# Performance work log

Hardware: AMD Instinct MI355X
Metric: run time of the kernel (lower is better)

## Reference

```python
import jax, jax.numpy as jnp
import numpy as np

EPS = 1e-5  # BatchNorm eps


def _add_self_loops(edge_index, num_nodes):
    loop = jnp.arange(num_nodes, dtype=edge_index.dtype)
    src = jnp.concatenate([edge_index[0], loop])
    dst = jnp.concatenate([edge_index[1], loop])
    return src, dst


def _gcn_conv(x, src, dst, norm, W, b, num_nodes):
    # PyG GCNConv: out = D^{-1/2} (A+I) D^{-1/2} (x W) + b
    h = x @ W                                # [N, out_dim]
    msg = h[src] * norm[:, None]             # [E+N, out_dim] gathered messages
    out = jax.ops.segment_sum(msg, dst, num_segments=num_nodes)
    return out + b


def _batch_norm(x, gamma, beta):
    # training-mode batch statistics over the node dimension (biased var)
    mean = jnp.mean(x, axis=0)
    var = jnp.var(x, axis=0)
    return (x - mean) * jax.lax.rsqrt(var + EPS) * gamma + beta


def setup_inputs() -> dict:
    key = jax.random.key(0)
    ks = jax.random.split(key, 10)
    N, E = 50000, 800000
    d_in, d_h, d_mid, d_out = 1536, 512, 128, 5

    x = jax.random.normal(ks[0], (N, d_in), dtype=jnp.float32)
    edge_index = jax.random.randint(ks[1], (2, E), 0, N, dtype=jnp.int32)

    def glorot(k, fan_in, fan_out):
        s = jnp.sqrt(6.0 / (fan_in + fan_out))
        return jax.random.uniform(k, (fan_in, fan_out), jnp.float32, -s, s)

    return {
        "x": x,
        "edge_index": edge_index,
        "W1": glorot(ks[2], d_in, d_h), "b1": jnp.zeros((d_h,), jnp.float32),
        "W2": glorot(ks[3], d_h, d_mid), "b2": jnp.zeros((d_mid,), jnp.float32),
        "W3": glorot(ks[4], d_mid, d_out), "b3": jnp.zeros((d_out,), jnp.float32),
        "gamma1": jnp.ones((d_h,), jnp.float32), "beta1": jnp.zeros((d_h,), jnp.float32),
        "gamma2": jnp.ones((d_mid,), jnp.float32), "beta2": jnp.zeros((d_mid,), jnp.float32),
    }


def reference(x, edge_index, W1, b1, W2, b2, W3, b3, gamma1, beta1, gamma2, beta2):
    N = x.shape[0]
    src, dst = _add_self_loops(edge_index, N)
    # symmetric degree normalization deg^{-1/2}[src] * deg^{-1/2}[dst]
    deg = jax.ops.segment_sum(jnp.ones_like(dst, dtype=x.dtype), dst, num_segments=N)
    inv_sqrt = jnp.where(deg > 0, jax.lax.rsqrt(deg), 0.0)
    norm = inv_sqrt[src] * inv_sqrt[dst]

    h = _gcn_conv(x, src, dst, norm, W1, b1, N)
    h = jax.nn.relu(_batch_norm(h, gamma1, beta1))  # dropout is identity in eval
    h = _gcn_conv(h, src, dst, norm, W2, b2, N)
    h = jax.nn.relu(_batch_norm(h, gamma2, beta2))
    h = _gcn_conv(h, src, dst, norm, W3, b3, N)
    return jax.nn.log_softmax(h, axis=1)
```

## Files before the change

kernel.cpp:

```cpp
#include <hip/hip_runtime.h>
#include <cstddef>
#include <cstdint>

typedef short s16x8 __attribute__((ext_vector_type(8)));
typedef unsigned short u16x4 __attribute__((ext_vector_type(4)));
typedef unsigned short u16x8 __attribute__((ext_vector_type(8)));
typedef float f32x4 __attribute__((ext_vector_type(4)));

__device__ __forceinline__ unsigned short f2bf(float f) {
  unsigned int u = __float_as_uint(f);
  u = (u + 0x7fffu + ((u >> 16) & 1u)) >> 16;
  return (unsigned short)u;
}
__device__ __forceinline__ float bf2f(unsigned short u) {
  return __uint_as_float(((unsigned int)u) << 16);
}

__device__ __forceinline__ void gl2lds16(const unsigned short* g, unsigned short* l) {
  __builtin_amdgcn_global_load_lds(
      (const __attribute__((address_space(1))) unsigned int*)g,
      (__attribute__((address_space(3))) unsigned int*)l, 16, 0, 0);
}
__device__ __forceinline__ void gl2lds16f(const float* g, float* l) {
  __builtin_amdgcn_global_load_lds(
      (const __attribute__((address_space(1))) unsigned int*)g,
      (__attribute__((address_space(3))) unsigned int*)l, 16, 0, 0);
}

static inline size_t alignup(size_t x) { return (x + 255) & ~(size_t)255; }

__global__ void count_kernel(const int* __restrict__ dst, int* __restrict__ counts, int E) {
  int e = blockIdx.x * blockDim.x + threadIdx.x;
  if (e < E) atomicAdd(&counts[dst[e]], 1);
}

__global__ void invsqrt_kernel(const int* __restrict__ counts, float* __restrict__ inv_s, int n) {
  int i = blockIdx.x * blockDim.x + threadIdx.x;
  if (i < n) inv_s[i] = rsqrtf((float)(counts[i] + 1));
}

__global__ void block_sum_kernel(const int* __restrict__ counts, int* __restrict__ bsum, int n) {
  __shared__ int red[256];
  int i = blockIdx.x * 256 + threadIdx.x;
  red[threadIdx.x] = (i < n) ? counts[i] : 0;
  __syncthreads();
  #pragma unroll
  for (int o = 128; o > 0; o >>= 1) {
    if (threadIdx.x < o) red[threadIdx.x] += red[threadIdx.x + o];
    __syncthreads();
  }
  if (threadIdx.x == 0) bsum[blockIdx.x] = red[0];
}

__global__ void scan_bsum_kernel(int* __restrict__ bsum, int nb) {
  __shared__ int s[256];
  int t = threadIdx.x;
  s[t] = (t < nb) ? bsum[t] : 0;
  __syncthreads();
  #pragma unroll
  for (int o = 1; o < 256; o <<= 1) {
    int v = (t >= o) ? s[t - o] : 0;
    __syncthreads();
    s[t] += v;
    __syncthreads();
  }
  if (t < nb) bsum[t] = (t == 0) ? 0 : s[t - 1];
}

__global__ void scan_apply_kernel(const int* __restrict__ counts, const int* __restrict__ bpre,
                                  int* __restrict__ offsets, int n) {
  __shared__ int s[256];
  int t = threadIdx.x;
  int i = blockIdx.x * 256 + t;
  s[t] = (i < n) ? counts[i] : 0;
  __syncthreads();
  #pragma unroll
  for (int o = 1; o < 256; o <<= 1) {
    int v = (t >= o) ? s[t - o] : 0;
    __syncthreads();
    s[t] += v;
    __syncthreads();
  }
  if (i < n) offsets[i + 1] = s[t] + bpre[blockIdx.x];
  if (i == 0) offsets[0] = 0;
}

__global__ void fill_kernel(const int* __restrict__ src, const int* __restrict__ dst,
                            const int* __restrict__ offsets, int* __restrict__ cursor,
                            int* __restrict__ csr_src, int E) {
  int e = blockIdx.x * blockDim.x + threadIdx.x;
  if (e >= E) return;
  int d = dst[e];
  int pos = atomicAdd(&cursor[d], 1);
  csr_src[offsets[d] + pos] = src[e];
}

__global__ void transpose_w_kernel(const float* __restrict__ W, unsigned short* __restrict__ Wt,
                                   int K, int N) {
  __shared__ float tile[32][33];
  int k0 = blockIdx.x * 32, n0 = blockIdx.y * 32;
  int tx = threadIdx.x & 31, ty = threadIdx.x >> 5;
  #pragma unroll
  for (int i = 0; i < 32; i += 8)
    tile[ty + i][tx] = W[(size_t)(k0 + ty + i) * N + n0 + tx];
  __syncthreads();
  #pragma unroll
  for (int i = 0; i < 32; i += 8)
    Wt[(size_t)(n0 + ty + i) * K + k0 + tx] = f2bf(tile[tx][ty + i]);
}

__global__ __launch_bounds__(512) void gemm1_kernel(
    const float* __restrict__ A, const unsigned short* __restrict__ B,
    unsigned short* __restrict__ C, int M) {
  __shared__ __align__(16) float As[2][128 * 32];
  __shared__ __align__(16) unsigned short Bs[2][256 * 32];
  const int K = 1536;
  const int NT = 48;
  int tid = threadIdx.x, lane = tid & 63, w = tid >> 6;

  int nwg = gridDim.x * gridDim.y;
  int orig = blockIdx.y * gridDim.x + blockIdx.x;
  int q = nwg >> 3, r = nwg & 7;
  int xcd = orig & 7, loc = orig >> 3;
  int wg = (xcd < r) ? xcd * (q + 1) + loc : r * (q + 1) + (xcd - r) * q + loc;
  int bx = wg & 1, by = wg >> 1;

  int m0 = by * 128, n0 = bx * 256;
  int wm = (w >> 2) * 64, wn = (w & 3) * 64;

  f32x4 acc[4][4];
  #pragma unroll
  for (int i = 0; i < 4; i++)
    #pragma unroll
    for (int j = 0; j < 4; j++) acc[i][j] = (f32x4){0.f, 0.f, 0.f, 0.f};

  int row0 = tid >> 3, slot0 = tid & 7;
  int row1 = 64 + row0;
  const float* agp0 = &A[(size_t)min(m0 + row0, M - 1) * K + ((slot0 ^ (row0 & 7)) << 2)];
  const float* agp1 = &A[(size_t)min(m0 + row1, M - 1) * K + ((slot0 ^ (row1 & 7)) << 2)];
  int adst0 = tid * 4, adst1 = (512 + tid) * 4;
  int brow = tid >> 2, bslot = tid & 3;
  int bsrc = (bslot ^ (brow & 3)) << 3;
  const unsigned short* bgp0 = &B[(size_t)(n0 + brow) * K + bsrc];
  const unsigned short* bgp1 = &B[(size_t)(n0 + 128 + brow) * K + bsrc];
  int bdst0 = tid * 8, bdst1 = (512 + tid) * 8;

  gl2lds16f(agp0, &As[0][adst0]);
  gl2lds16f(agp1, &As[0][adst1]);
  gl2lds16(bgp0, &Bs[0][bdst0]);
  gl2lds16(bgp1, &Bs[0][bdst1]);
  __syncthreads();

  int cur = 0;
  for (int t = 0; t < NT; t++) {
    if (t + 1 < NT) {
      int kb = (t + 1) * 32;
      gl2lds16f(agp0 + kb, &As[cur ^ 1][adst0]);
      gl2lds16f(agp1 + kb, &As[cur ^ 1][adst1]);
      gl2lds16(bgp0 + kb, &Bs[cur ^ 1][bdst0]);
      gl2lds16(bgp1 + kb, &Bs[cur ^ 1][bdst1]);
    }
    int jc = lane >> 4;
    s16x8 af[4], bfr[4];
    #pragma unroll
    for (int i = 0; i < 4; i++) {
      int rr = wm + i * 16 + (lane & 15);
      f32x4 v0 = *reinterpret_cast<const f32x4*>(
          &As[cur][rr * 32 + ((((2 * jc) ^ (rr & 7))) << 2)]);
      f32x4 v1 = *reinterpret_cast<const f32x4*>(
          &As[cur][rr * 32 + ((((2 * jc + 1) ^ (rr & 7))) << 2)]);
      unsigned int c0, c1, c2, c3;
      asm("v_cvt_pk_bf16_f32 %0, %1, %2" : "=v"(c0) : "v"(v0[0]), "v"(v0[1]));
      asm("v_cvt_pk_bf16_f32 %0, %1, %2" : "=v"(c1) : "v"(v0[2]), "v"(v0[3]));
      asm("v_cvt_pk_bf16_f32 %0, %1, %2" : "=v"(c2) : "v"(v1[0]), "v"(v1[1]));
      asm("v_cvt_pk_bf16_f32 %0, %1, %2" : "=v"(c3) : "v"(v1[2]), "v"(v1[3]));
      uint4 pk;
      pk.x = c0; pk.y = c1; pk.z = c2; pk.w = c3;
      af[i] = __builtin_bit_cast(s16x8, pk);
      int rn = wn + i * 16 + (lane & 15);
      bfr[i] = *reinterpret_cast<const s16x8*>(&Bs[cur][rn * 32 + ((jc ^ (rn & 3)) << 3)]);
    }
    #pragma unroll
    for (int i = 0; i < 4; i++)
      #pragma unroll
      for (int j = 0; j < 4; j++)
        acc[i][j] = __builtin_amdgcn_mfma_f32_16x16x32_bf16(af[i], bfr[j], acc[i][j], 0, 0, 0);
    __syncthreads();
    cur ^= 1;
  }

  #pragma unroll
  for (int i = 0; i < 4; i++) {
    #pragma unroll
    for (int j = 0; j < 4; j++) {
      int col = n0 + wn + j * 16 + (lane & 15);
      #pragma unroll
      for (int r2 = 0; r2 < 4; r2++) {
        int row = m0 + wm + i * 16 + (lane >> 4) * 4 + r2;
        if (row < M) C[(size_t)row * 512 + col] = f2bf(acc[i][j][r2]);
      }
    }
  }
}

#define LDT 72
__global__ __launch_bounds__(256) void gemm2_kernel(
    const unsigned short* __restrict__ A, const unsigned short* __restrict__ Bt,
    const float* __restrict__ sc, const float* __restrict__ sh,
    unsigned short* __restrict__ C, int M) {
  const int N = 128, K = 512;
  __shared__ unsigned short As[64 * LDT];
  __shared__ unsigned short Bs[128 * LDT];
  int tid = threadIdx.x;
  int m0 = blockIdx.y * 64;
  int w = tid >> 6, lane = tid & 63;
  int wm = (w >> 1) * 32, wn = (w & 1) * 64;

  f32x4 acc[2][4];
  #pragma unroll
  for (int i = 0; i < 2; i++)
    #pragma unroll
    for (int j = 0; j < 4; j++) acc[i][j] = (f32x4){0.f, 0.f, 0.f, 0.f};

  for (int k0 = 0; k0 < K; k0 += 64) {
    #pragma unroll
    for (int r = 0; r < 2; r++) {
      int idx = r * 256 + tid;
      int row = idx >> 3;
      int seg = (idx & 7) * 8;
      int gr = m0 + row;
      u16x8 v = (u16x8){0, 0, 0, 0, 0, 0, 0, 0};
      if (gr < M) v = *reinterpret_cast<const u16x8*>(&A[(size_t)gr * K + k0 + seg]);
      int c = k0 + seg;
      u16x8 p;
      #pragma unroll
      for (int j = 0; j < 8; j++) {
        float f = fmaxf(bf2f(v[j]) * sc[c + j] + sh[c + j], 0.f);
        p[j] = f2bf(f);
      }
      *reinterpret_cast<u16x8*>(&As[row * LDT + seg]) = p;
    }
    #pragma unroll
    for (int r = 0; r < 4; r++) {
      int idx = r * 256 + tid;
      int n = idx >> 3;
      int seg = (idx & 7) * 8;
      u16x8 v = *reinterpret_cast<const u16x8*>(&Bt[(size_t)n * K + k0 + seg]);
      *reinterpret_cast<u16x8*>(&Bs[n * LDT + seg]) = v;
    }
    __syncthreads();
    #pragma unroll
    for (int ks = 0; ks < 2; ks++) {
      s16x8 af[2], bfr[4];
      #pragma unroll
      for (int i = 0; i < 2; i++)
        af[i] = *reinterpret_cast<const s16x8*>(
            &As[(wm + i * 16 + (lane & 15)) * LDT + ks * 32 + (lane >> 4) * 8]);
      #pragma unroll
      for (int j = 0; j < 4; j++)
        bfr[j] = *reinterpret_cast<const s16x8*>(
            &Bs[(wn + j * 16 + (lane & 15)) * LDT + ks * 32 + (lane >> 4) * 8]);
      #pragma unroll
      for (int i = 0; i < 2; i++)
        #pragma unroll
        for (int j = 0; j < 4; j++)
          acc[i][j] = __builtin_amdgcn_mfma_f32_16x16x32_bf16(af[i], bfr[j], acc[i][j], 0, 0, 0);
    }
    __syncthreads();
  }
  #pragma unroll
  for (int i = 0; i < 2; i++) {
    #pragma unroll
    for (int j = 0; j < 4; j++) {
      int col = wn + j * 16 + (lane & 15);
      #pragma unroll
      for (int r = 0; r < 4; r++) {
        int row = m0 + wm + i * 16 + (lane >> 4) * 4 + r;
        if (row < M) C[(size_t)row * N + col] = f2bf(acc[i][j][r]);
      }
    }
  }
}

__global__ void agg512_kernel(const unsigned short* __restrict__ h, const int* __restrict__ offsets,
                              const int* __restrict__ csr, const float* __restrict__ inv_s,
                              unsigned short* __restrict__ out, int n) {
  int wv = threadIdx.x >> 6, lane = threadIdx.x & 63;
  int node = blockIdx.x * 4 + wv;
  if (node >= n) return;
  const u16x8* h8 = reinterpret_cast<const u16x8*>(h);
  float di = inv_s[node];
  size_t rb = (size_t)node * 64;
  float acc[8];
  u16x8 v0 = h8[rb + lane];
  float dd = di * di;
  #pragma unroll
  for (int j = 0; j < 8; j++) acc[j] = bf2f(v0[j]) * dd;
  int e = offsets[node], e1 = offsets[node + 1];
  for (; e + 1 < e1; e += 2) {
    int sA = csr[e], sB = csr[e + 1];
    float wA = inv_s[sA] * di, wB = inv_s[sB] * di;
    u16x8 vA = h8[(size_t)sA * 64 + lane];
    u16x8 vB = h8[(size_t)sB * 64 + lane];
    #pragma unroll
    for (int j = 0; j < 8; j++) acc[j] += bf2f(vA[j]) * wA + bf2f(vB[j]) * wB;
  }
  if (e < e1) {
    int sA = csr[e];
    float wA = inv_s[sA] * di;
    u16x8 vA = h8[(size_t)sA * 64 + lane];
    #pragma unroll
    for (int j = 0; j < 8; j++) acc[j] += bf2f(vA[j]) * wA;
  }
  u16x8 o;
  #pragma unroll
  for (int j = 0; j < 8; j++) o[j] = f2bf(acc[j]);
  reinterpret_cast<u16x8*>(out)[rb + lane] = o;
}

__global__ void agg128_kernel(const unsigned short* __restrict__ h, const int* __restrict__ offsets,
                              const int* __restrict__ csr, const float* __restrict__ inv_s,
                              unsigned short* __restrict__ out, int n) {
  int wv = threadIdx.x >> 6, lane = threadIdx.x & 63;
  int node = blockIdx.x * 4 + wv;
  if (node >= n) return;
  const unsigned int* h2 = reinterpret_cast<const unsigned int*>(h);
  float di = inv_s[node];
  size_t rb = (size_t)node * 64;
  unsigned int u0 = h2[rb + lane];
  float dd = di * di;
  float alo = __uint_as_float(u0 << 16) * dd;
  float ahi = __uint_as_float(u0 & 0xffff0000u) * dd;
  int e = offsets[node], e1 = offsets[node + 1];
  for (; e + 1 < e1; e += 2) {
    int sA = csr[e], sB = csr[e + 1];
    float wA = inv_s[sA] * di, wB = inv_s[sB] * di;
    unsigned int uA = h2[(size_t)sA * 64 + lane];
    unsigned int uB = h2[(size_t)sB * 64 + lane];
    alo += __uint_as_float(uA << 16) * wA + __uint_as_float(uB << 16) * wB;
    ahi += __uint_as_float(uA & 0xffff0000u) * wA + __uint_as_float(uB & 0xffff0000u) * wB;
  }
  if (e < e1) {
    int sA = csr[e];
    float wA = inv_s[sA] * di;
    unsigned int uA = h2[(size_t)sA * 64 + lane];
    alo += __uint_as_float(uA << 16) * wA;
    ahi += __uint_as_float(uA & 0xffff0000u) * wA;
  }
  unsigned int uo = ((unsigned int)f2bf(ahi) << 16) | (unsigned int)f2bf(alo);
  reinterpret_cast<unsigned int*>(out)[rb + lane] = uo;
}

__global__ void bn_stats512_kernel(const unsigned short* __restrict__ x, float* __restrict__ accum,
                                   int nrows, int rpb) {
  int r0 = blockIdx.x * rpb, r1 = min(nrows, r0 + rpb);
  int t = threadIdx.x;
  const unsigned int* x2 = reinterpret_cast<const unsigned int*>(x);
  float s0 = 0.f, q0 = 0.f, s1 = 0.f, q1 = 0.f;
  for (int r = r0; r < r1; r++) {
    unsigned int u = x2[(size_t)r * 256 + t];
    float lo = __uint_as_float(u << 16);
    float hi = __uint_as_float(u & 0xffff0000u);
    s0 += lo; q0 += lo * lo; s1 += hi; q1 += hi * hi;
  }
  atomicAdd(&accum[2 * t], s0);
  atomicAdd(&accum[2 * t + 1], s1);
  atomicAdd(&accum[512 + 2 * t], q0);
  atomicAdd(&accum[512 + 2 * t + 1], q1);
}

__global__ void bn_stats128_kernel(const unsigned short* __restrict__ x, float* __restrict__ accum,
                                   int nrows, int rpb) {
  int r0 = blockIdx.x * rpb, r1 = min(nrows, r0 + rpb);
  int t = threadIdx.x;
  int colu = t & 63, rofs = t >> 6;
  const unsigned int* x2 = reinterpret_cast<const unsigned int*>(x);
  float s0 = 0.f, q0 = 0.f, s1 = 0.f, q1 = 0.f;
  for (int r = r0 + rofs; r < r1; r += 4) {
    unsigned int u = x2[(size_t)r * 64 + colu];
    float lo = __uint_as_float(u << 16);
    float hi = __uint_as_float(u & 0xffff0000u);
    s0 += lo; q0 += lo * lo; s1 += hi; q1 += hi * hi;
  }
  atomicAdd(&accum[2 * colu], s0);
  atomicAdd(&accum[2 * colu + 1], s1);
  atomicAdd(&accum[128 + 2 * colu], q0);
  atomicAdd(&accum[128 + 2 * colu + 1], q1);
}

__global__ void bn_finalize_kernel(const float* __restrict__ accum, const float* __restrict__ gamma,
                                   const float* __restrict__ beta, float* __restrict__ scale,
                                   float* __restrict__ shift, int D, float invN) {
  int c = blockIdx.x * blockDim.x + threadIdx.x;
  if (c >= D) return;
  float mean = accum[c] * invN;
  float var = accum[D + c] * invN - mean * mean;
  float sc = gamma[c] * rsqrtf(var + 1e-5f);
  scale[c] = sc;
  shift[c] = beta[c] - mean * sc;
}

__global__ void gemm3_kernel(const unsigned short* __restrict__ A, const float* __restrict__ W,
                             const float* __restrict__ sc, const float* __restrict__ sh,
                             float* __restrict__ C, int M) {
  __shared__ float Ws[128 * 5];
  __shared__ float scs[128], shs[128];
  int tid = threadIdx.x;
  for (int i = tid; i < 128 * 5; i += blockDim.x) Ws[i] = W[i];
  if (tid < 128) { scs[tid] = sc[tid]; shs[tid] = sh[tid]; }
  __syncthreads();
  int row = blockIdx.x * blockDim.x + tid;
  if (row >= M) return;
  float acc[5] = {0.f, 0.f, 0.f, 0.f, 0.f};
  const u16x8* a8 = reinterpret_cast<const u16x8*>(A + (size_t)row * 128);
  for (int k8 = 0; k8 < 16; k8++) {
    u16x8 v = a8[k8];
    int k = k8 * 8;
    #pragma unroll
    for (int j = 0; j < 8; j++) {
      float f = fmaxf(bf2f(v[j]) * scs[k + j] + shs[k + j], 0.f);
      #pragma unroll
      for (int c = 0; c < 5; c++) acc[c] += f * Ws[(k + j) * 5 + c];
    }
  }
  #pragma unroll
  for (int j = 0; j < 5; j++) C[(size_t)row * 5 + j] = acc[j];
}

__global__ void agg3_lsm_kernel(const float* __restrict__ h, const int* __restrict__ offsets,
                                const int* __restrict__ csr, const float* __restrict__ inv_s,
                                const float* __restrict__ b3, float* __restrict__ out, int n) {
  int node = blockIdx.x * blockDim.x + threadIdx.x;
  if (node >= n) return;
  float di = inv_s[node];
  float acc[5];
  #pragma unroll
  for (int j = 0; j < 5; j++) acc[j] = h[(size_t)node * 5 + j] * di * di;
  int s0 = offsets[node], s1 = offsets[node + 1];
  for (int e = s0; e < s1; e++) {
    int s = csr[e];
    float wgt = inv_s[s] * di;
    #pragma unroll
    for (int j = 0; j < 5; j++) acc[j] += h[(size_t)s * 5 + j] * wgt;
  }
  #pragma unroll
  for (int j = 0; j < 5; j++) acc[j] += b3[j];
  float m = acc[0];
  #pragma unroll
  for (int j = 1; j < 5; j++) m = fmaxf(m, acc[j]);
  float sum = 0.f;
  #pragma unroll
  for (int j = 0; j < 5; j++) sum += expf(acc[j] - m);
  float lse = logf(sum);
  #pragma unroll
  for (int j = 0; j < 5; j++) out[(size_t)node * 5 + j] = acc[j] - m - lse;
}

extern "C" void kernel_launch(void* const* d_in, const int* in_sizes, int n_in,
                              void* d_out, int out_size, void* d_ws, size_t ws_size,
                              hipStream_t stream) {
  const float* x      = (const float*)d_in[0];
  const int*   ei     = (const int*)d_in[1];
  const float* W1     = (const float*)d_in[2];
  const float* b3     = (const float*)d_in[7];
  const float* W2     = (const float*)d_in[4];
  const float* W3     = (const float*)d_in[6];
  const float* gamma1 = (const float*)d_in[8];
  const float* beta1  = (const float*)d_in[9];
  const float* gamma2 = (const float*)d_in[10];
  const float* beta2  = (const float*)d_in[11];

  const int N = in_sizes[0] / 1536;
  const int E = in_sizes[1] / 2;
  const int* src = ei;
  const int* dst = ei + E;

  const int mblocks = (N + 127) / 128;
  const int Mpad = mblocks * 128;
  const int nb = (N + 255) / 256;

  char* ws = (char*)d_ws;
  size_t szRA = alignup((size_t)N * 512 * sizeof(float));
  size_t szXB = alignup((size_t)Mpad * 1536 * sizeof(unsigned short));
  char* RAb = ws;
  char* RBb = ws + szRA;
  char* sp = ws + szRA + szXB;
  int* counts   = (int*)sp;           sp += alignup((size_t)N * 4);
  int* cursor   = (int*)sp;           sp += alignup((size_t)N * 4);
  int* offsets  = (int*)sp;           sp += alignup((size_t)(N + 1) * 4);
  int* csr_src  = (int*)sp;           sp += alignup((size_t)E * 4);
  float* inv_s  = (float*)sp;         sp += alignup((size_t)N * 4);
  unsigned short* W1t = (unsigned short*)sp; sp += alignup((size_t)512 * 1536 * 2);
  unsigned short* W2t = (unsigned short*)sp; sp += alignup((size_t)128 * 512 * 2);
  float* accum  = (float*)sp;         sp += alignup(1024 * 4);
  float* sc1    = (float*)sp;         sp += alignup(512 * 4);
  float* sh1    = (float*)sp;         sp += alignup(512 * 4);
  float* sc2    = (float*)sp;         sp += alignup(128 * 4);
  float* sh2    = (float*)sp;         sp += alignup(128 * 4);
  int* bsum     = (int*)sp;           sp += alignup(256 * 4);

  unsigned short* H1  = (unsigned short*)RAb;
  unsigned short* G1  = (unsigned short*)RBb;
  unsigned short* H2  = (unsigned short*)RAb;
  unsigned short* G2  = (unsigned short*)RBb;
  float*          H3  = (float*)RAb;

  hipMemsetAsync(counts, 0, (size_t)N * 4, stream);
  hipMemsetAsync(cursor, 0, (size_t)N * 4, stream);
  count_kernel<<<(E + 255) / 256, 256, 0, stream>>>(dst, counts, E);
  invsqrt_kernel<<<(N + 255) / 256, 256, 0, stream>>>(counts, inv_s, N);
  block_sum_kernel<<<nb, 256, 0, stream>>>(counts, bsum, N);
  scan_bsum_kernel<<<1, 256, 0, stream>>>(bsum, nb);
  scan_apply_kernel<<<nb, 256, 0, stream>>>(counts, bsum, offsets, N);
  fill_kernel<<<(E + 255) / 256, 256, 0, stream>>>(src, dst, offsets, cursor, csr_src, E);

  transpose_w_kernel<<<dim3(1536 / 32, 512 / 32), 256, 0, stream>>>(W1, W1t, 1536, 512);
  transpose_w_kernel<<<dim3(512 / 32, 128 / 32), 256, 0, stream>>>(W2, W2t, 512, 128);

  int aggblocks = (N + 3) / 4;
  int rpb = (N + 511) / 512;

  gemm1_kernel<<<dim3(2, mblocks), 512, 0, stream>>>(x, W1t, H1, N);
  agg512_kernel<<<aggblocks, 256, 0, stream>>>(H1, offsets, csr_src, inv_s, G1, N);
  hipMemsetAsync(accum, 0, 1024 * 4, stream);
  bn_stats512_kernel<<<512, 256, 0, stream>>>(G1, accum, N, rpb);
  bn_finalize_kernel<<<2, 256, 0, stream>>>(accum, gamma1, beta1, sc1, sh1, 512, 1.0f / N);

  gemm2_kernel<<<dim3(1, (N + 63) / 64), 256, 0, stream>>>(G1, W2t, sc1, sh1, H2, N);
  agg128_kernel<<<aggblocks, 256, 0, stream>>>(H2, offsets, csr_src, inv_s, G2, N);
  hipMemsetAsync(accum, 0, 1024 * 4, stream);
  bn_stats128_kernel<<<512, 256, 0, stream>>>(G2, accum, N, rpb);
  bn_finalize_kernel<<<1, 256, 0, stream>>>(accum, gamma2, beta2, sc2, sh2, 128, 1.0f / N);

  gemm3_kernel<<<(N + 255) / 256, 256, 0, stream>>>(G2, W3, sc2, sh2, H3, N);
  agg3_lsm_kernel<<<(N + 255) / 256, 256, 0, stream>>>(H3, offsets, csr_src, inv_s, b3,
                                                       (float*)d_out, N);
}
```

Baseline: 665.2 us.

## Triple-buffer gemm1 LDS pipeline with partial vmcnt waits and new B layout

```diff
diff --git a/kernel.cpp b/kernel.cpp
--- a/kernel.cpp
+++ b/kernel.cpp
@@ -112,10 +112,9 @@
 __global__ __launch_bounds__(512) void gemm1_kernel(
     const float* __restrict__ A, const unsigned short* __restrict__ B,
     unsigned short* __restrict__ C, int M) {
-  __shared__ __align__(16) float As[2][128 * 32];
-  __shared__ __align__(16) unsigned short Bs[2][256 * 32];
+  __shared__ __align__(16) float As[3][128 * 32];
+  __shared__ __align__(16) unsigned short Bs[3][256 * 32];
   const int K = 1536;
-  const int NT = 48;
   int tid = threadIdx.x, lane = tid & 63, w = tid >> 6;
 
   int nwg = gridDim.x * gridDim.y;
@@ -139,36 +138,27 @@
   const float* agp0 = &A[(size_t)min(m0 + row0, M - 1) * K + ((slot0 ^ (row0 & 7)) << 2)];
   const float* agp1 = &A[(size_t)min(m0 + row1, M - 1) * K + ((slot0 ^ (row1 & 7)) << 2)];
   int adst0 = tid * 4, adst1 = (512 + tid) * 4;
-  int brow = tid >> 2, bslot = tid & 3;
-  int bsrc = (bslot ^ (brow & 3)) << 3;
-  const unsigned short* bgp0 = &B[(size_t)(n0 + brow) * K + bsrc];
-  const unsigned short* bgp1 = &B[(size_t)(n0 + 128 + brow) * K + bsrc];
-  int bdst0 = tid * 8, bdst1 = (512 + tid) * 8;
-
-  gl2lds16f(agp0, &As[0][adst0]);
-  gl2lds16f(agp1, &As[0][adst1]);
-  gl2lds16(bgp0, &Bs[0][bdst0]);
-  gl2lds16(bgp1, &Bs[0][bdst1]);
-  __syncthreads();
-
-  int cur = 0;
-  for (int t = 0; t < NT; t++) {
-    if (t + 1 < NT) {
-      int kb = (t + 1) * 32;
-      gl2lds16f(agp0 + kb, &As[cur ^ 1][adst0]);
-      gl2lds16f(agp1 + kb, &As[cur ^ 1][adst1]);
-      gl2lds16(bgp0 + kb, &Bs[cur ^ 1][bdst0]);
-      gl2lds16(bgp1 + kb, &Bs[cur ^ 1][bdst1]);
-    }
+  int E0 = tid, E1 = 512 + tid;
+  int brow0 = ((E0 >> 5) << 3) + (E0 & 7), bslot0 = ((E0 >> 3) & 3) ^ (E0 & 3);
+  int brow1 = ((E1 >> 5) << 3) + (E1 & 7), bslot1 = ((E1 >> 3) & 3) ^ (E1 & 3);
+  const unsigned short* bg0 = &B[(size_t)(n0 + brow0) * K + bslot0 * 8];
+  const unsigned short* bg1 = &B[(size_t)(n0 + brow1) * K + bslot1 * 8];
+  int bdst0 = E0 * 8, bdst1 = E1 * 8;
+
+  auto stage = [&](int kb, float* AsW, unsigned short* BsW) {
+    gl2lds16f(agp0 + kb, AsW + adst0);
+    gl2lds16f(agp1 + kb, AsW + adst1);
+    gl2lds16(bg0 + kb, BsW + bdst0);
+    gl2lds16(bg1 + kb, BsW + bdst1);
+  };
+  auto mfma_phase = [&](const float* AsR, const unsigned short* BsR) {
     int jc = lane >> 4;
     s16x8 af[4], bfr[4];
     #pragma unroll
     for (int i = 0; i < 4; i++) {
       int rr = wm + i * 16 + (lane & 15);
-      f32x4 v0 = *reinterpret_cast<const f32x4*>(
-          &As[cur][rr * 32 + ((((2 * jc) ^ (rr & 7))) << 2)]);
-      f32x4 v1 = *reinterpret_cast<const f32x4*>(
-          &As[cur][rr * 32 + ((((2 * jc + 1) ^ (rr & 7))) << 2)]);
+      f32x4 v0 = *reinterpret_cast<const f32x4*>(&AsR[rr * 32 + (((2 * jc) ^ (rr & 7)) << 2)]);
+      f32x4 v1 = *reinterpret_cast<const f32x4*>(&AsR[rr * 32 + (((2 * jc + 1) ^ (rr & 7)) << 2)]);
       unsigned int c0, c1, c2, c3;
       asm("v_cvt_pk_bf16_f32 %0, %1, %2" : "=v"(c0) : "v"(v0[0]), "v"(v0[1]));
       asm("v_cvt_pk_bf16_f32 %0, %1, %2" : "=v"(c1) : "v"(v0[2]), "v"(v0[3]));
@@ -178,16 +168,44 @@
       pk.x = c0; pk.y = c1; pk.z = c2; pk.w = c3;
       af[i] = __builtin_bit_cast(s16x8, pk);
       int rn = wn + i * 16 + (lane & 15);
-      bfr[i] = *reinterpret_cast<const s16x8*>(&Bs[cur][rn * 32 + ((jc ^ (rn & 3)) << 3)]);
+      int be = ((rn >> 3) << 5) + (((jc ^ (rn & 3)) & 3) << 3) + (rn & 7);
+      bfr[i] = *reinterpret_cast<const s16x8*>(&BsR[be * 8]);
     }
     #pragma unroll
     for (int i = 0; i < 4; i++)
       #pragma unroll
       for (int j = 0; j < 4; j++)
         acc[i][j] = __builtin_amdgcn_mfma_f32_16x16x32_bf16(af[i], bfr[j], acc[i][j], 0, 0, 0);
-    __syncthreads();
-    cur ^= 1;
-  }
+  };
+
+  stage(0, As[0], Bs[0]);
+  stage(32, As[1], Bs[1]);
+  asm volatile("s_waitcnt vmcnt(4)" ::: "memory");
+  __builtin_amdgcn_s_barrier();
+
+  for (int t = 0; t < 45; t += 3) {
+    int kb = t * 32;
+    stage(kb + 64, As[2], Bs[2]);
+    mfma_phase(As[0], Bs[0]);
+    asm volatile("s_waitcnt lgkmcnt(0) vmcnt(4)" ::: "memory");
+    __builtin_amdgcn_s_barrier();
+    stage(kb + 96, As[0], Bs[0]);
+    mfma_phase(As[1], Bs[1]);
+    asm volatile("s_waitcnt lgkmcnt(0) vmcnt(4)" ::: "memory");
+    __builtin_amdgcn_s_barrier();
+    stage(kb + 128, As[1], Bs[1]);
+    mfma_phase(As[2], Bs[2]);
+    asm volatile("s_waitcnt lgkmcnt(0) vmcnt(4)" ::: "memory");
+    __builtin_amdgcn_s_barrier();
+  }
+  stage(47 * 32, As[2], Bs[2]);
+  mfma_phase(As[0], Bs[0]);
+  asm volatile("s_waitcnt lgkmcnt(0) vmcnt(4)" ::: "memory");
+  __builtin_amdgcn_s_barrier();
+  mfma_phase(As[1], Bs[1]);
+  asm volatile("s_waitcnt lgkmcnt(0) vmcnt(0)" ::: "memory");
+  __builtin_amdgcn_s_barrier();
+  mfma_phase(As[2], Bs[2]);
 
   #pragma unroll
   for (int i = 0; i < 4; i++) {
```

After: 700.2 us. 5.3% more time.
